# Kernel optimization log

Measured on AMD Instinct MI355X. Metric: run time of the kernel, lower is better.

Reference implementation:

```python
import math
import jax, jax.numpy as jnp
import numpy as np

N_LAYER = 4
N_HEAD = 16
N_EMBD = 1024
HEAD_DIM = N_EMBD // N_HEAD
VOCAB = 4096
EPS = 1e-5

def _alibi_slopes(n_heads):
    def pow2(n):
        start = 2.0 ** (-2.0 ** (-(math.log2(n) - 3)))
        return [start * start ** i for i in range(n)]
    if n_heads & (n_heads - 1) == 0:
        s = pow2(n_heads)
    else:
        c = 2 ** math.floor(math.log2(n_heads))
        s = pow2(c)
        eb = 2.0 ** (-2.0 ** (-(math.log2(2 * c) - 3)))
        s += [eb * eb ** i for i in range(n_heads - c)]
        s = s[:n_heads]
    return jnp.asarray(np.array(s, dtype=np.float32))

SLOPES = _alibi_slopes(N_HEAD)  # [H]

def _alibi_bias(T):
    pos = jnp.arange(T, dtype=jnp.float32)
    rel = pos[None, :] - pos[:, None]                      # j - i
    bias = SLOPES[:, None, None] * rel[None, :, :]          # [H,T,T]
    causal = pos[None, :] <= pos[:, None]                   # [T,T] lower-tri
    return jnp.where(causal[None, :, :], bias, -jnp.inf)

def _sym_ln(x, w, b):
    # per-head LayerNorm over head_dim, scaled/shifted per head
    B, T, C = x.shape
    xh = x.reshape(B, T, N_HEAD, HEAD_DIM)
    mu = xh.mean(-1, keepdims=True)
    var = ((xh - mu) ** 2).mean(-1, keepdims=True)
    nh = (xh - mu) / jnp.sqrt(var + EPS)
    nh = nh * w[None, None, :, None] + b[None, None, :, None]
    return nh.reshape(B, T, C)

def _attn(x, caw, cab, cpw, cpb):
    B, T, C = x.shape
    qkv = x @ caw.T + cab                                    # [B,T,3C]
    q, k, v = jnp.split(qkv, 3, axis=-1)
    q = q.reshape(B, T, N_HEAD, HEAD_DIM)
    k = k.reshape(B, T, N_HEAD, HEAD_DIM)
    v = v.reshape(B, T, N_HEAD, HEAD_DIM)
    scale = 1.0 / math.sqrt(HEAD_DIM)
    scores = jnp.einsum('bthd,bshd->bhts', q, k) * scale     # [B,H,T,T]
    scores = scores + _alibi_bias(T)[None]
    w = jax.nn.softmax(scores, axis=-1)
    y = jnp.einsum('bhts,bshd->bthd', w, v).reshape(B, T, C)
    return y @ cpw.T + cpb

def _vocab_ffn(x, wte, fw, fb, temps):
    B, T, C = x.shape
    xh = x.reshape(B, T, N_HEAD, HEAD_DIM)
    f = xh @ fw.T + fb                                       # shared per-channel FFN
    vc = wte.reshape(VOCAB, N_HEAD, HEAD_DIM).transpose(1, 0, 2)  # [H,V,D]
    logits = jnp.einsum('bthd,hvd->bthv', f, vc)
    t = jnp.maximum(temps, 0.1)[None, None, :, None]
    w = jax.nn.softmax(logits / t, axis=-1)
    out = jnp.einsum('bthv,hvd->bthd', w, vc)
    return out.reshape(B, T, C)

def _forward(idx, wte, c_attn_w, c_attn_b, c_proj_w, c_proj_b, ffn_w, ffn_b,
             temps, ln1_w, ln1_b, ln2_w, ln2_b, lnf_w, lnf_b):
    x = wte[idx]                                             # [B,T,C]
    for l in range(N_LAYER):
        x = x + _attn(_sym_ln(x, ln1_w[l], ln1_b[l]),
                      c_attn_w[l], c_attn_b[l], c_proj_w[l], c_proj_b[l])
        x = x + _vocab_ffn(_sym_ln(x, ln2_w[l], ln2_b[l]),
                           wte, ffn_w[l], ffn_b[l], temps[l])
    x = _sym_ln(x, lnf_w, lnf_b)
    return x @ wte.T                                         # tied lm head logits


def setup_inputs() -> dict:
    key = jax.random.key(0)
    ks = jax.random.split(key, 8)
    B, T = 2, 1024
    return {
        'idx': jax.random.randint(ks[0], (B, T), 0, VOCAB),
        'wte': jax.random.normal(ks[1], (VOCAB, N_EMBD), jnp.float32) * 0.02,
        'c_attn_w': jax.random.normal(ks[2], (N_LAYER, 3 * N_EMBD, N_EMBD), jnp.float32) * 0.02,
        'c_attn_b': jnp.zeros((N_LAYER, 3 * N_EMBD), jnp.float32),
        'c_proj_w': jax.random.normal(ks[3], (N_LAYER, N_EMBD, N_EMBD), jnp.float32) * 0.02,
        'c_proj_b': jnp.zeros((N_LAYER, N_EMBD), jnp.float32),
        'ffn_w': jax.random.normal(ks[4], (N_LAYER, HEAD_DIM, HEAD_DIM), jnp.float32) * 0.02,
        'ffn_b': jnp.zeros((N_LAYER, HEAD_DIM), jnp.float32),
        'temps': jnp.ones((N_LAYER, N_HEAD), jnp.float32),
        'ln1_w': jnp.ones((N_LAYER, N_HEAD), jnp.float32),
        'ln1_b': jnp.zeros((N_LAYER, N_HEAD), jnp.float32),
        'ln2_w': jnp.ones((N_LAYER, N_HEAD), jnp.float32),
        'ln2_b': jnp.zeros((N_LAYER, N_HEAD), jnp.float32),
        'lnf_w': jnp.ones((N_HEAD,), jnp.float32),
        'lnf_b': jnp.zeros((N_HEAD,), jnp.float32),
    }


def reference(idx, wte, c_attn_w, c_attn_b, c_proj_w, c_proj_b, ffn_w, ffn_b,
              temps, ln1_w, ln1_b, ln2_w, ln2_b, lnf_w, lnf_b):
    return _forward(idx, wte, c_attn_w, c_attn_b, c_proj_w, c_proj_b, ffn_w, ffn_b,
                    temps, ln1_w, ln1_b, ln2_w, ln2_b, lnf_w, lnf_b)
```

## Files before the change

kernel.cpp:

```cpp
#include <hip/hip_runtime.h>

#define CDIM 1024
#define NHEAD 16
#define HD 64
#define NVOC 4096
#define TLEN 1024

typedef float4 f4;
typedef unsigned short ushort_t;
typedef __attribute__((ext_vector_type(8))) short short8;
typedef __attribute__((ext_vector_type(4))) short short4v;
typedef __attribute__((ext_vector_type(4))) float f32x4;
typedef __attribute__((ext_vector_type(2))) unsigned int uint2v;

#define SWZB(row, bcol) ((((row) << 7) + (bcol)) ^ (((row) & 7) << 4))

__device__ __forceinline__ ushort_t f2b(float x) {
  union { float f; unsigned u; } v; v.f = x;
  unsigned r = v.u + 0x7FFFu + ((v.u >> 16) & 1u);
  return (ushort_t)(r >> 16);
}
__device__ __forceinline__ short8 ldsr8(const ushort_t* b, int row, int bcol) {
  return *(const short8*)((const char*)b + SWZB(row, bcol));
}
__device__ __forceinline__ void ldsw8(ushort_t* b, int row, int bcol, short8 v) {
  *(short8*)((char*)b + SWZB(row, bcol)) = v;
}
__device__ __forceinline__ void ldswu2(ushort_t* b, int row, int bcol, uint2v v) {
  *(uint2v*)((char*)b + SWZB(row, bcol)) = v;
}
__device__ __forceinline__ void ldsw4(ushort_t* b, int row, int bcol, short4v v) {
  *(short4v*)((char*)b + SWZB(row, bcol)) = v;
}
__device__ __forceinline__ void ldsw1(ushort_t* b, int row, int bcol, ushort_t v) {
  *(ushort_t*)((char*)b + SWZB(row, bcol)) = v;
}
__device__ __forceinline__ ushort_t ldsr1(const ushort_t* b, int row, int bcol) {
  return *(const ushort_t*)((const char*)b + SWZB(row, bcol));
}
__device__ __forceinline__ unsigned cvtpk(float lo, float hi) {
  unsigned r;
  asm("v_cvt_pk_bf16_f32 %0, %1, %2" : "=v"(r) : "v"(lo), "v"(hi));
  return r;
}

__global__ __launch_bounds__(256) void k_cvt(const float* __restrict__ in,
                                             ushort_t* __restrict__ out) {
  size_t i = ((size_t)blockIdx.x * 256 + threadIdx.x) * 8;
  f4 a = *(const f4*)(in + i);
  f4 b = *(const f4*)(in + i + 4);
  short8 o = {(short)f2b(a.x), (short)f2b(a.y), (short)f2b(a.z), (short)f2b(a.w),
              (short)f2b(b.x), (short)f2b(b.y), (short)f2b(b.z), (short)f2b(b.w)};
  *(short8*)(out + i) = o;
}

__global__ __launch_bounds__(256) void k_embed(const int* __restrict__ idx,
                                               const float* __restrict__ wte,
                                               float* __restrict__ x) {
  int row = blockIdx.x;
  int tok = idx[row];
  const f4* s = reinterpret_cast<const f4*>(wte + (size_t)tok * CDIM);
  f4* d = reinterpret_cast<f4*>(x + (size_t)row * CDIM);
  d[threadIdx.x] = s[threadIdx.x];
}

__global__ __launch_bounds__(256) void k_symln(const float* __restrict__ in,
                                               ushort_t* __restrict__ out,
                                               const float* __restrict__ w,
                                               const float* __restrict__ b) {
  int gw = blockIdx.x * 4 + (threadIdx.x >> 6);
  int lane = threadIdx.x & 63;
  int row = gw >> 4, h = gw & 15;
  int off = row * CDIM + h * HD + lane;
  float v = in[off];
  float s = v;
#pragma unroll
  for (int o = 32; o; o >>= 1) s += __shfl_xor(s, o);
  float mu = s * (1.0f / HD);
  float d = v - mu;
  float q = d * d;
#pragma unroll
  for (int o = 32; o; o >>= 1) q += __shfl_xor(q, o);
  float nh = d * rsqrtf(q * (1.0f / HD) + 1e-5f);
  out[off] = f2b(nh * w[h] + b[h]);
}

__global__ __launch_bounds__(256) void k_gemm_bf(const ushort_t* __restrict__ A,
                                                 const ushort_t* __restrict__ B,
                                                 const float* __restrict__ bias,
                                                 const float* __restrict__ res,
                                                 float* __restrict__ C,
                                                 ushort_t* __restrict__ Cbf,
                                                 int M, int N, int K) {
  __shared__ ushort_t sA[128 * 64];
  __shared__ ushort_t sB[128 * 64];
  const int tid = threadIdx.x;
  const int bn = blockIdx.x * 128, bm = blockIdx.y * 128;
  const int w = tid >> 6, lane = tid & 63;
  const int c = lane & 15, g = lane >> 4;
  const int wr = (w >> 1) * 64, wc = (w & 1) * 64;
  const int srow = tid >> 1, sseg = tid & 1;
  const ushort_t* Ap = A + (size_t)(bm + srow) * K + sseg * 32;
  const ushort_t* Bp = B + (size_t)(bn + srow) * K + sseg * 32;
  const f32x4 Z = {0.f, 0.f, 0.f, 0.f};
  f32x4 acc[4][4];
#pragma unroll
  for (int fm = 0; fm < 4; ++fm)
#pragma unroll
    for (int fn = 0; fn < 4; ++fn) acc[fm][fn] = Z;

  short8 ra[4], rb[4];
#pragma unroll
  for (int j = 0; j < 4; ++j) {
    ra[j] = *(const short8*)(Ap + j * 8);
    rb[j] = *(const short8*)(Bp + j * 8);
  }
  const int NT = K >> 6;
  for (int kt = 0; kt < NT; ++kt) {
    __syncthreads();
#pragma unroll
    for (int j = 0; j < 4; ++j) {
      ldsw8(sA, srow, sseg * 64 + j * 16, ra[j]);
      ldsw8(sB, srow, sseg * 64 + j * 16, rb[j]);
    }
    __syncthreads();
    if (kt + 1 < NT) {
      const ushort_t* An = Ap + (kt + 1) * 64;
      const ushort_t* Bn = Bp + (kt + 1) * 64;
#pragma unroll
      for (int j = 0; j < 4; ++j) {
        ra[j] = *(const short8*)(An + j * 8);
        rb[j] = *(const short8*)(Bn + j * 8);
      }
    }
#pragma unroll
    for (int ch = 0; ch < 2; ++ch) {
      short8 bfr[4];
#pragma unroll
      for (int fn = 0; fn < 4; ++fn) bfr[fn] = ldsr8(sB, wc + fn * 16 + c, ch * 64 + g * 16);
#pragma unroll
      for (int fm = 0; fm < 4; ++fm) {
        short8 afr = ldsr8(sA, wr + fm * 16 + c, ch * 64 + g * 16);
#pragma unroll
        for (int fn = 0; fn < 4; ++fn)
          acc[fm][fn] = __builtin_amdgcn_mfma_f32_16x16x32_bf16(afr, bfr[fn], acc[fm][fn], 0, 0, 0);
      }
    }
  }
#pragma unroll
  for (int fm = 0; fm < 4; ++fm) {
#pragma unroll
    for (int reg = 0; reg < 4; ++reg) {
      int row = bm + wr + fm * 16 + g * 4 + reg;
#pragma unroll
      for (int fn = 0; fn < 4; ++fn) {
        int col = bn + wc + fn * 16 + c;
        float v = acc[fm][fn][reg];
        if (bias) v += bias[col];
        if (res) v += res[(size_t)row * N + col];
        if (Cbf) Cbf[(size_t)row * N + col] = f2b(v);
        else     C[(size_t)row * N + col] = v;
      }
    }
  }
}

__global__ __launch_bounds__(256) void k_prep_vt(const ushort_t* __restrict__ qkv,
                                                 ushort_t* __restrict__ vt) {
  __shared__ ushort_t t[64 * 64];
  const int h = blockIdx.x, tt = blockIdx.y, b = blockIdx.z;
  const int tid = threadIdx.x;
  {
    int r = tid >> 2, seg = tid & 3;
    const short8* src = (const short8*)(qkv + (size_t)(b * TLEN + tt * 64 + r) * (3 * CDIM)
                                        + 2 * CDIM + h * HD + seg * 16);
    ldsw8(t, r, seg * 32, src[0]);
    ldsw8(t, r, seg * 32 + 16, src[1]);
  }
  __syncthreads();
  {
    int dr = tid >> 2, vs = tid & 3;
    ushort_t vals[16];
#pragma unroll
    for (int j = 0; j < 16; ++j) vals[j] = ldsr1(t, vs * 16 + j, dr * 2);
    short8 w1 = {(short)vals[0], (short)vals[1], (short)vals[2], (short)vals[3],
                 (short)vals[4], (short)vals[5], (short)vals[6], (short)vals[7]};
    short8 w2 = {(short)vals[8], (short)vals[9], (short)vals[10], (short)vals[11],
                 (short)vals[12], (short)vals[13], (short)vals[14], (short)vals[15]};
    ushort_t* dst = vt + (size_t)b * CDIM * TLEN + (size_t)(h * HD + dr) * TLEN + tt * 64 + vs * 16;
    *(short8*)dst = w1;
    *(short8*)(dst + 8) = w2;
  }
}

__global__ __launch_bounds__(512) void k_flash_mfma(const ushort_t* __restrict__ qkv,
                                                    const ushort_t* __restrict__ vt,
                                                    ushort_t* __restrict__ y) {
  __shared__ ushort_t sK[64 * 64];
  __shared__ ushort_t sVt[64 * 64];
  __shared__ ushort_t sP[128 * 64];
  const int qt = blockIdx.x, h = blockIdx.y, b = blockIdx.z;
  const int tid = threadIdx.x;
  const int w = tid >> 6, lane = tid & 63;
  const int c = lane & 15, g = lane >> 4;
  const int row0 = qt * 128;
  const f32x4 Z = {0.f, 0.f, 0.f, 0.f};
  const float k1 = 0.125f * 1.4426950408889634f;
  const float slope2 = exp2f(-0.5f * (float)(h + 1)) * 1.4426950408889634f;

  short8 qf[2];
  {
    const ushort_t* qrow = qkv + (size_t)(b * TLEN + row0 + w * 16 + c) * (3 * CDIM) + h * HD;
    qf[0] = *(const short8*)(qrow + g * 8);
    qf[1] = *(const short8*)(qrow + 32 + g * 8);
  }

  const int sr = tid >> 3, sc8 = tid & 7;
  const ushort_t* kbase = qkv + (size_t)(b * TLEN + sr) * (3 * CDIM) + CDIM + h * HD + sc8 * 8;
  const ushort_t* vbase = vt + (size_t)b * CDIM * TLEN + (size_t)(h * HD + sr) * TLEN + sc8 * 8;
  short8 pk = *(const short8*)kbase;
  short8 pv = *(const short8*)vbase;

  float lrun = 0.f;
  f32x4 oacc[4] = {Z, Z, Z, Z};
  const int NT = 2 * qt + 2;

  for (int kt = 0; kt < NT; ++kt) {
    const int kb = kt * 64;
    __syncthreads();
    ldsw8(sK, sr, sc8 * 16, pk);
    ldsw8(sVt, sr, sc8 * 16, pv);
    __syncthreads();
    if (kt + 1 < NT) {
      pk = *(const short8*)(kbase + (size_t)(kb + 64) * (3 * CDIM));
      pv = *(const short8*)(vbase + kb + 64);
    }
    f32x4 sacc[4] = {Z, Z, Z, Z};
#pragma unroll
    for (int ch = 0; ch < 2; ++ch) {
#pragma unroll
      for (int vf = 0; vf < 4; ++vf) {
        short8 af = ldsr8(sK, vf * 16 + c, ch * 64 + g * 16);
        sacc[vf] = __builtin_amdgcn_mfma_f32_16x16x32_bf16(af, qf[ch], sacc[vf], 0, 0, 0);
      }
    }
    const int ibase = kb + g * 4 - (row0 + w * 16 + c);
    const float fbase = (float)ibase;
    float ssum = 0.f;
#pragma unroll
    for (int vf = 0; vf < 4; ++vf) {
      float p[4];
#pragma unroll
      for (int reg = 0; reg < 4; ++reg) {
        float s = fmaf(slope2, fbase + (float)(vf * 16 + reg), sacc[vf][reg] * k1);
        p[reg] = (ibase + vf * 16 + reg <= 0) ? exp2f(s) : 0.f;
        ssum += p[reg];
      }
      short4v pq = {(short)f2b(p[0]), (short)f2b(p[1]), (short)f2b(p[2]), (short)f2b(p[3])};
      ldsw4(sP, w * 16 + c, (vf * 16 + g * 4) * 2, pq);
    }
    ssum += __shfl_xor(ssum, 16);
    ssum += __shfl_xor(ssum, 32);
    lrun += ssum;
#pragma unroll
    for (int ch = 0; ch < 2; ++ch) {
      short8 af = ldsr8(sP, w * 16 + c, ch * 64 + g * 16);
#pragma unroll
      for (int nf = 0; nf < 4; ++nf) {
        short8 bfv = ldsr8(sVt, nf * 16 + c, ch * 64 + g * 16);
        oacc[nf] = __builtin_amdgcn_mfma_f32_16x16x32_bf16(af, bfv, oacc[nf], 0, 0, 0);
      }
    }
  }
  float linv = 1.0f / lrun;
#pragma unroll
  for (int reg = 0; reg < 4; ++reg) {
    float li = __shfl(linv, g * 4 + reg);
    int row = b * TLEN + row0 + w * 16 + g * 4 + reg;
#pragma unroll
    for (int nf = 0; nf < 4; ++nf) {
      y[(size_t)row * CDIM + h * HD + nf * 16 + c] = f2b(oacc[nf][reg] * li);
    }
  }
}

__global__ __launch_bounds__(256) void k_prep_wt(const float* __restrict__ wte,
                                                 ushort_t* __restrict__ wt) {
  __shared__ ushort_t t[64 * 64];
  const int h = blockIdx.x, vt = blockIdx.y;
  const int tid = threadIdx.x;
  {
    int r = tid >> 2, seg = tid & 3;
    const f4* src = (const f4*)(wte + (size_t)(vt * 64 + r) * CDIM + h * HD + seg * 16);
    f4 a = src[0], b = src[1], c2 = src[2], d2 = src[3];
    short8 o1 = {(short)f2b(a.x), (short)f2b(a.y), (short)f2b(a.z), (short)f2b(a.w),
                 (short)f2b(b.x), (short)f2b(b.y), (short)f2b(b.z), (short)f2b(b.w)};
    short8 o2 = {(short)f2b(c2.x), (short)f2b(c2.y), (short)f2b(c2.z), (short)f2b(c2.w),
                 (short)f2b(d2.x), (short)f2b(d2.y), (short)f2b(d2.z), (short)f2b(d2.w)};
    ldsw8(t, r, seg * 32, o1);
    ldsw8(t, r, seg * 32 + 16, o2);
  }
  __syncthreads();
  {
    int dr = tid >> 2, vs = tid & 3;
    ushort_t vals[16];
#pragma unroll
    for (int j = 0; j < 16; ++j) vals[j] = ldsr1(t, vs * 16 + j, dr * 2);
    short8 w1 = {(short)vals[0], (short)vals[1], (short)vals[2], (short)vals[3],
                 (short)vals[4], (short)vals[5], (short)vals[6], (short)vals[7]};
    short8 w2 = {(short)vals[8], (short)vals[9], (short)vals[10], (short)vals[11],
                 (short)vals[12], (short)vals[13], (short)vals[14], (short)vals[15]};
    ushort_t* dst = wt + (size_t)(h * 64 + dr) * NVOC + vt * 64 + vs * 16;
    *(short8*)dst = w1;
    *(short8*)(dst + 8) = w2;
  }
}

__global__ __launch_bounds__(256) void k_vocab_mfma(
    const ushort_t* __restrict__ ln2, const float* __restrict__ fw,
    const float* __restrict__ fb, const float* __restrict__ temps,
    const ushort_t* __restrict__ wb, const ushort_t* __restrict__ wt,
    float* __restrict__ x) {
  __shared__ ushort_t sW[64 * 64];
  __shared__ ushort_t sWt[64 * 64];
  __shared__ ushort_t sF[64 * 64];
  __shared__ ushort_t sP[64 * 64];
  const int h = blockIdx.x, rt = blockIdx.y;
  const int tid = threadIdx.x;
  const int w = tid >> 6, lane = tid & 63;
  const int c = lane & 15, g = lane >> 4;
  const int row0 = rt * 64;
  const f32x4 Z = {0.f, 0.f, 0.f, 0.f};

  {
    int r = tid >> 2, seg = tid & 3;
    const short8* src = (const short8*)(ln2 + (size_t)(row0 + r) * CDIM + h * HD + seg * 16);
    ldsw8(sP, r, seg * 32, src[0]);
    ldsw8(sP, r, seg * 32 + 16, src[1]);
    const f4* src2 = (const f4*)(fw + r * HD + seg * 16);
    f4 a = src2[0], b = src2[1], c2 = src2[2], d2 = src2[3];
    short8 o1 = {(short)f2b(a.x), (short)f2b(a.y), (short)f2b(a.z), (short)f2b(a.w),
                 (short)f2b(b.x), (short)f2b(b.y), (short)f2b(b.z), (short)f2b(b.w)};
    short8 o2 = {(short)f2b(c2.x), (short)f2b(c2.y), (short)f2b(c2.z), (short)f2b(c2.w),
                 (short)f2b(d2.x), (short)f2b(d2.y), (short)f2b(d2.z), (short)f2b(d2.w)};
    ldsw8(sW, r, seg * 32, o1);
    ldsw8(sW, r, seg * 32 + 16, o2);
  }
  __syncthreads();

  const float invt_l2e = (1.0f / fmaxf(temps[h], 0.1f)) * 1.4426950408889634f;
  {
    f32x4 facc[4] = {Z, Z, Z, Z};
#pragma unroll
    for (int ch = 0; ch < 2; ++ch) {
      short8 af = ldsr8(sP, w * 16 + c, ch * 64 + g * 16);
#pragma unroll
      for (int nf = 0; nf < 4; ++nf) {
        short8 bf = ldsr8(sW, nf * 16 + c, ch * 64 + g * 16);
        facc[nf] = __builtin_amdgcn_mfma_f32_16x16x32_bf16(af, bf, facc[nf], 0, 0, 0);
      }
    }
    __syncthreads();
#pragma unroll
    for (int nf = 0; nf < 4; ++nf) {
      float fbv = fb[nf * 16 + c];
#pragma unroll
      for (int reg = 0; reg < 4; ++reg) {
        float val = (facc[nf][reg] + fbv) * invt_l2e;
        ldsw1(sF, w * 16 + g * 4 + reg, (nf * 16 + c) * 2, f2b(val));
      }
    }
  }

  const int sr = tid >> 2, sc4 = tid & 3;
  const size_t gw_base = (size_t)sr * CDIM + h * HD + sc4 * 16;
  const size_t gt_base = (size_t)(h * 64 + sr) * NVOC + sc4 * 16;
  short8 pw0 = *(const short8*)(wb + gw_base);
  short8 pw1 = *(const short8*)(wb + gw_base + 8);
  short8 pt0 = *(const short8*)(wt + gt_base);
  short8 pt1 = *(const short8*)(wt + gt_base + 8);

  float lrun = 0.f;
  f32x4 oacc[4] = {Z, Z, Z, Z};

  for (int vt = 0; vt < 64; ++vt) {
    __syncthreads();
    ldsw8(sW, sr, sc4 * 32, pw0);
    ldsw8(sW, sr, sc4 * 32 + 16, pw1);
    ldsw8(sWt, sr, sc4 * 32, pt0);
    ldsw8(sWt, sr, sc4 * 32 + 16, pt1);
    __syncthreads();
    if (vt < 63) {
      size_t go = gw_base + (size_t)(vt + 1) * 64 * CDIM;
      pw0 = *(const short8*)(wb + go);
      pw1 = *(const short8*)(wb + go + 8);
      size_t gt = gt_base + (size_t)(vt + 1) * 64;
      pt0 = *(const short8*)(wt + gt);
      pt1 = *(const short8*)(wt + gt + 8);
    }
    f32x4 sacc[4] = {Z, Z, Z, Z};
#pragma unroll
    for (int ch = 0; ch < 2; ++ch) {
      short8 bfq = ldsr8(sF, w * 16 + c, ch * 64 + g * 16);
#pragma unroll
      for (int vf = 0; vf < 4; ++vf) {
        short8 af = ldsr8(sW, vf * 16 + c, ch * 64 + g * 16);
        sacc[vf] = __builtin_amdgcn_mfma_f32_16x16x32_bf16(af, bfq, sacc[vf], 0, 0, 0);
      }
    }
    float ssum = 0.f;
#pragma unroll
    for (int vf = 0; vf < 4; ++vf) {
      float p0 = exp2f(sacc[vf][0]);
      float p1 = exp2f(sacc[vf][1]);
      float p2 = exp2f(sacc[vf][2]);
      float p3 = exp2f(sacc[vf][3]);
      ssum += (p0 + p1) + (p2 + p3);
      uint2v pq = {cvtpk(p0, p1), cvtpk(p2, p3)};
      ldswu2(sP, w * 16 + c, (vf * 16 + g * 4) * 2, pq);
    }
    ssum += __shfl_xor(ssum, 16);
    ssum += __shfl_xor(ssum, 32);
    lrun += ssum;
#pragma unroll
    for (int ch = 0; ch < 2; ++ch) {
      short8 af = ldsr8(sP, w * 16 + c, ch * 64 + g * 16);
#pragma unroll
      for (int nf = 0; nf < 4; ++nf) {
        short8 bfv = ldsr8(sWt, nf * 16 + c, ch * 64 + g * 16);
        oacc[nf] = __builtin_amdgcn_mfma_f32_16x16x32_bf16(af, bfv, oacc[nf], 0, 0, 0);
      }
    }
  }
  float linv = 1.0f / lrun;
#pragma unroll
  for (int reg = 0; reg < 4; ++reg) {
    float li = __shfl(linv, g * 4 + reg);
    int row = row0 + w * 16 + g * 4 + reg;
#pragma unroll
    for (int nf = 0; nf < 4; ++nf) {
      float* xp = x + (size_t)row * CDIM + h * HD + nf * 16 + c;
      *xp += oacc[nf][reg] * li;
    }
  }
}

extern "C" void kernel_launch(void* const* d_in, const int* in_sizes, int n_in,
                              void* d_out, int out_size, void* d_ws, size_t ws_size,
                              hipStream_t stream) {
  const int*   idx   = (const int*)  d_in[0];
  const float* wte   = (const float*)d_in[1];
  const float* caw   = (const float*)d_in[2];
  const float* cab   = (const float*)d_in[3];
  const float* cpw   = (const float*)d_in[4];
  const float* cpb   = (const float*)d_in[5];
  const float* ffw   = (const float*)d_in[6];
  const float* ffb   = (const float*)d_in[7];
  const float* temps = (const float*)d_in[8];
  const float* l1w   = (const float*)d_in[9];
  const float* l1b   = (const float*)d_in[10];
  const float* l2w   = (const float*)d_in[11];
  const float* l2b   = (const float*)d_in[12];
  const float* lfw   = (const float*)d_in[13];
  const float* lfb   = (const float*)d_in[14];
  float* out = (float*)d_out;

  char* P = (char*)d_ws;
  float*    x      = (float*)P;
  ushort_t* qkv_bf = (ushort_t*)(P + 8388608);
  ushort_t* ln_bf  = (ushort_t*)(P + 20971520);
  ushort_t* yb_bf  = (ushort_t*)(P + 25165824);
  ushort_t* vtb    = (ushort_t*)(P + 29360128);
  ushort_t* caw_bf = (ushort_t*)(P + 33554432);
  ushort_t* wb     = (ushort_t*)(P + 58720256);
  ushort_t* wt     = (ushort_t*)d_out;
  ushort_t* cpw_bf = (ushort_t*)d_out + 4194304;

  k_cvt<<<6144, 256, 0, stream>>>(caw, caw_bf);
  k_cvt<<<2048, 256, 0, stream>>>(cpw, cpw_bf);
  k_cvt<<<2048, 256, 0, stream>>>(wte, wb);
  k_prep_wt<<<dim3(16, 64), 256, 0, stream>>>(wte, wt);
  k_embed<<<2048, 256, 0, stream>>>(idx, wte, x);
  for (int l = 0; l < 4; ++l) {
    k_symln<<<8192, 256, 0, stream>>>(x, ln_bf, l1w + l * 16, l1b + l * 16);
    k_gemm_bf<<<dim3(24, 16), 256, 0, stream>>>(ln_bf, caw_bf + (size_t)l * 3072 * 1024,
                                                cab + l * 3072, nullptr, nullptr, qkv_bf,
                                                2048, 3072, 1024);
    k_prep_vt<<<dim3(16, 16, 2), 256, 0, stream>>>(qkv_bf, vtb);
    k_flash_mfma<<<dim3(8, 16, 2), 512, 0, stream>>>(qkv_bf, vtb, yb_bf);
    k_gemm_bf<<<dim3(8, 16), 256, 0, stream>>>(yb_bf, cpw_bf + (size_t)l * 1024 * 1024,
                                               cpb + l * 1024, x, x, nullptr,
                                               2048, 1024, 1024);
    k_symln<<<8192, 256, 0, stream>>>(x, ln_bf, l2w + l * 16, l2b + l * 16);
    k_vocab_mfma<<<dim3(16, 32), 256, 0, stream>>>(ln_bf, ffw + l * 4096, ffb + l * 64,
                                                   temps + l * 16, wb, wt, x);
  }
  k_symln<<<8192, 256, 0, stream>>>(x, ln_bf, lfw, lfb);
  k_gemm_bf<<<dim3(32, 16), 256, 0, stream>>>(ln_bf, wb, nullptr, nullptr, out, nullptr,
                                              2048, 4096, 1024);
}
```

Before: 998.8 us.

## Pre-swizzle vocab weights into MFMA fragment order and load directly to registers

A new prep kernel writes the bf16 vocab embedding and its transpose in per-lane MFMA fragment order. The vocab attention kernel can then load its A/B operands straight from global memory into registers. This drops the shared-memory staging buffer for the transposed weights and the two barriers per vocab tile, and the F-operand fragments are hoisted out of the loop. In exchange, each of the four waves now fetches the full weight tile itself, which raises L2 traffic. The explicit next-tile register prefetch is also gone, so global load latency may be exposed inside the loop.

```diff
diff --git a/kernel.cpp b/kernel.cpp
--- a/kernel.cpp
+++ b/kernel.cpp
@@ -284,45 +284,45 @@
   }
 }
 
-__global__ __launch_bounds__(256) void k_prep_wt(const float* __restrict__ wte,
-                                                 ushort_t* __restrict__ wt) {
-  __shared__ ushort_t t[64 * 64];
-  const int h = blockIdx.x, vt = blockIdx.y;
+__global__ __launch_bounds__(256) void k_prep_frag(const float* __restrict__ wte,
+                                                   ushort_t* __restrict__ wfrag,
+                                                   ushort_t* __restrict__ wtfrag) {
+  const int h = blockIdx.x, vtile = blockIdx.y;
   const int tid = threadIdx.x;
-  {
-    int r = tid >> 2, seg = tid & 3;
-    const f4* src = (const f4*)(wte + (size_t)(vt * 64 + r) * CDIM + h * HD + seg * 16);
-    f4 a = src[0], b = src[1], c2 = src[2], d2 = src[3];
-    short8 o1 = {(short)f2b(a.x), (short)f2b(a.y), (short)f2b(a.z), (short)f2b(a.w),
-                 (short)f2b(b.x), (short)f2b(b.y), (short)f2b(b.z), (short)f2b(b.w)};
-    short8 o2 = {(short)f2b(c2.x), (short)f2b(c2.y), (short)f2b(c2.z), (short)f2b(c2.w),
-                 (short)f2b(d2.x), (short)f2b(d2.y), (short)f2b(d2.z), (short)f2b(d2.w)};
-    ldsw8(t, r, seg * 32, o1);
-    ldsw8(t, r, seg * 32 + 16, o2);
-  }
-  __syncthreads();
-  {
-    int dr = tid >> 2, vs = tid & 3;
-    ushort_t vals[16];
-#pragma unroll
-    for (int j = 0; j < 16; ++j) vals[j] = ldsr1(t, vs * 16 + j, dr * 2);
-    short8 w1 = {(short)vals[0], (short)vals[1], (short)vals[2], (short)vals[3],
-                 (short)vals[4], (short)vals[5], (short)vals[6], (short)vals[7]};
-    short8 w2 = {(short)vals[8], (short)vals[9], (short)vals[10], (short)vals[11],
-                 (short)vals[12], (short)vals[13], (short)vals[14], (short)vals[15]};
-    ushort_t* dst = wt + (size_t)(h * 64 + dr) * NVOC + vt * 64 + vs * 16;
-    *(short8*)dst = w1;
-    *(short8*)(dst + 8) = w2;
+  for (int p = tid; p < 1024; p += 256) {
+    int s = p >> 6, l = p & 63;
+    int cc = l & 15, gg = l >> 4;
+    ushort_t tmp[8];
+    ushort_t* dst;
+    if (s < 8) {
+      int vf = s >> 1, ch = s & 1;
+      const float* src = wte + (size_t)(vtile * 64 + vf * 16 + cc) * CDIM + h * HD + ch * 32 + gg * 8;
+      f4 a = *(const f4*)src;
+      f4 b = *(const f4*)(src + 4);
+      tmp[0] = f2b(a.x); tmp[1] = f2b(a.y); tmp[2] = f2b(a.z); tmp[3] = f2b(a.w);
+      tmp[4] = f2b(b.x); tmp[5] = f2b(b.y); tmp[6] = f2b(b.z); tmp[7] = f2b(b.w);
+      dst = wfrag + (((size_t)(h * 64 + vtile) * 8 + s) * 512) + l * 8;
+    } else {
+      int s2 = s - 8;
+      int nf = s2 >> 1, ch = s2 & 1;
+      int rowb = vtile * 64 + ch * 32 + gg * 8;
+      int col = h * HD + nf * 16 + cc;
+#pragma unroll
+      for (int j = 0; j < 8; ++j) tmp[j] = f2b(wte[(size_t)(rowb + j) * CDIM + col]);
+      dst = wtfrag + (((size_t)(h * 64 + vtile) * 8 + s2) * 512) + l * 8;
+    }
+    short8 o = {(short)tmp[0], (short)tmp[1], (short)tmp[2], (short)tmp[3],
+                (short)tmp[4], (short)tmp[5], (short)tmp[6], (short)tmp[7]};
+    *(short8*)dst = o;
   }
 }
 
 __global__ __launch_bounds__(256) void k_vocab_mfma(
     const ushort_t* __restrict__ ln2, const float* __restrict__ fw,
     const float* __restrict__ fb, const float* __restrict__ temps,
-    const ushort_t* __restrict__ wb, const ushort_t* __restrict__ wt,
+    const ushort_t* __restrict__ wfrag, const ushort_t* __restrict__ wtfrag,
     float* __restrict__ x) {
   __shared__ ushort_t sW[64 * 64];
-  __shared__ ushort_t sWt[64 * 64];
   __shared__ ushort_t sF[64 * 64];
   __shared__ ushort_t sP[64 * 64];
   const int h = blockIdx.x, rt = blockIdx.y;
@@ -349,6 +349,7 @@
   __syncthreads();
 
   const float invt_l2e = (1.0f / fmaxf(temps[h], 0.1f)) * 1.4426950408889634f;
+  short8 bfq[2];
   {
     f32x4 facc[4] = {Z, Z, Z, Z};
 #pragma unroll
@@ -360,7 +361,6 @@
         facc[nf] = __builtin_amdgcn_mfma_f32_16x16x32_bf16(af, bf, facc[nf], 0, 0, 0);
       }
     }
-    __syncthreads();
 #pragma unroll
     for (int nf = 0; nf < 4; ++nf) {
       float fbv = fb[nf * 16 + c];
@@ -370,44 +370,31 @@
         ldsw1(sF, w * 16 + g * 4 + reg, (nf * 16 + c) * 2, f2b(val));
       }
     }
-  }
-
-  const int sr = tid >> 2, sc4 = tid & 3;
-  const size_t gw_base = (size_t)sr * CDIM + h * HD + sc4 * 16;
-  const size_t gt_base = (size_t)(h * 64 + sr) * NVOC + sc4 * 16;
-  short8 pw0 = *(const short8*)(wb + gw_base);
-  short8 pw1 = *(const short8*)(wb + gw_base + 8);
-  short8 pt0 = *(const short8*)(wt + gt_base);
-  short8 pt1 = *(const short8*)(wt + gt_base + 8);
+    bfq[0] = ldsr8(sF, w * 16 + c, g * 16);
+    bfq[1] = ldsr8(sF, w * 16 + c, 64 + g * 16);
+  }
+
+  const ushort_t* wfp = wfrag + (size_t)h * 64 * 8 * 512 + lane * 8;
+  const ushort_t* wtp = wtfrag + (size_t)h * 64 * 8 * 512 + lane * 8;
 
   float lrun = 0.f;
   f32x4 oacc[4] = {Z, Z, Z, Z};
 
   for (int vt = 0; vt < 64; ++vt) {
-    __syncthreads();
-    ldsw8(sW, sr, sc4 * 32, pw0);
-    ldsw8(sW, sr, sc4 * 32 + 16, pw1);
-    ldsw8(sWt, sr, sc4 * 32, pt0);
-    ldsw8(sWt, sr, sc4 * 32 + 16, pt1);
-    __syncthreads();
-    if (vt < 63) {
-      size_t go = gw_base + (size_t)(vt + 1) * 64 * CDIM;
-      pw0 = *(const short8*)(wb + go);
-      pw1 = *(const short8*)(wb + go + 8);
-      size_t gt = gt_base + (size_t)(vt + 1) * 64;
-      pt0 = *(const short8*)(wt + gt);
-      pt1 = *(const short8*)(wt + gt + 8);
+    const ushort_t* ap = wfp + (size_t)vt * 4096;
+    const ushort_t* bp = wtp + (size_t)vt * 4096;
+    short8 wf[8], wtf[8];
+#pragma unroll
+    for (int s = 0; s < 8; ++s) {
+      wf[s] = *(const short8*)(ap + s * 512);
+      wtf[s] = *(const short8*)(bp + s * 512);
     }
     f32x4 sacc[4] = {Z, Z, Z, Z};
 #pragma unroll
-    for (int ch = 0; ch < 2; ++ch) {
-      short8 bfq = ldsr8(sF, w * 16 + c, ch * 64 + g * 16);
-#pragma unroll
-      for (int vf = 0; vf < 4; ++vf) {
-        short8 af = ldsr8(sW, vf * 16 + c, ch * 64 + g * 16);
-        sacc[vf] = __builtin_amdgcn_mfma_f32_16x16x32_bf16(af, bfq, sacc[vf], 0, 0, 0);
-      }
-    }
+    for (int ch = 0; ch < 2; ++ch)
+#pragma unroll
+      for (int vf = 0; vf < 4; ++vf)
+        sacc[vf] = __builtin_amdgcn_mfma_f32_16x16x32_bf16(wf[vf * 2 + ch], bfq[ch], sacc[vf], 0, 0, 0);
     float ssum = 0.f;
 #pragma unroll
     for (int vf = 0; vf < 4; ++vf) {
@@ -426,10 +413,8 @@
     for (int ch = 0; ch < 2; ++ch) {
       short8 af = ldsr8(sP, w * 16 + c, ch * 64 + g * 16);
 #pragma unroll
-      for (int nf = 0; nf < 4; ++nf) {
-        short8 bfv = ldsr8(sWt, nf * 16 + c, ch * 64 + g * 16);
-        oacc[nf] = __builtin_amdgcn_mfma_f32_16x16x32_bf16(af, bfv, oacc[nf], 0, 0, 0);
-      }
+      for (int nf = 0; nf < 4; ++nf)
+        oacc[nf] = __builtin_amdgcn_mfma_f32_16x16x32_bf16(af, wtf[nf * 2 + ch], oacc[nf], 0, 0, 0);
     }
   }
   float linv = 1.0f / lrun;
@@ -473,13 +458,14 @@
   ushort_t* vtb    = (ushort_t*)(P + 29360128);
   ushort_t* caw_bf = (ushort_t*)(P + 33554432);
   ushort_t* wb     = (ushort_t*)(P + 58720256);
-  ushort_t* wt     = (ushort_t*)d_out;
+  ushort_t* wtfrag = (ushort_t*)d_out;
   ushort_t* cpw_bf = (ushort_t*)d_out + 4194304;
+  ushort_t* wfrag  = (ushort_t*)d_out + 8388608;
 
   k_cvt<<<6144, 256, 0, stream>>>(caw, caw_bf);
   k_cvt<<<2048, 256, 0, stream>>>(cpw, cpw_bf);
   k_cvt<<<2048, 256, 0, stream>>>(wte, wb);
-  k_prep_wt<<<dim3(16, 64), 256, 0, stream>>>(wte, wt);
+  k_prep_frag<<<dim3(16, 64), 256, 0, stream>>>(wte, wfrag, wtfrag);
   k_embed<<<2048, 256, 0, stream>>>(idx, wte, x);
   for (int l = 0; l < 4; ++l) {
     k_symln<<<8192, 256, 0, stream>>>(x, ln_bf, l1w + l * 16, l1b + l * 16);
@@ -493,7 +479,7 @@
                                                2048, 1024, 1024);
     k_symln<<<8192, 256, 0, stream>>>(x, ln_bf, l2w + l * 16, l2b + l * 16);
     k_vocab_mfma<<<dim3(16, 32), 256, 0, stream>>>(ln_bf, ffw + l * 4096, ffb + l * 64,
-                                                   temps + l * 16, wb, wt, x);
+                                                   temps + l * 16, wfrag, wtfrag, x);
   }
   k_symln<<<8192, 256, 0, stream>>>(x, ln_bf, lfw, lfb);
   k_gemm_bf<<<dim3(32, 16), 256, 0, stream>>>(ln_bf, wb, nullptr, nullptr, out, nullptr,
```

After: 957.2 us. 4.2% less time.
